# Kernel tuning notes

Measured on AMD Instinct MI355X. Metric: run time of the kernel, lower is better.

Reference implementation:

```python
import jax, jax.numpy as jnp
import numpy as np

H = 512

def setup_inputs() -> dict:
    key = jax.random.key(0)
    k1, k2, k3, k4 = jax.random.split(key, 4)
    B, S_dec, S_enc = 8, 2048, 2048
    encoder_output = jax.random.normal(k1, (B, S_enc, H), dtype=jnp.float32)
    decoder_output = jax.random.normal(k2, (B, S_dec, H), dtype=jnp.float32)
    # nn.Bilinear(H, H, 1): weight [1, H, H], bias [1]; init U(-1/sqrt(H), 1/sqrt(H))
    bound = 1.0 / np.sqrt(H)
    W = jax.random.uniform(k3, (1, H, H), dtype=jnp.float32, minval=-bound, maxval=bound)
    b = jax.random.uniform(k4, (1,), dtype=jnp.float32, minval=-bound, maxval=bound)
    return {"encoder_output": encoder_output, "decoder_output": decoder_output, "W": W, "b": b}

def reference(encoder_output, decoder_output, W, b):
    # Original: scores[b,d,e] = Bilinear(enc[b,e], dec[b,d]) = enc[b,e] @ W[0] @ dec[b,d] + bias
    # Computed as two GEMMs instead of expanding to [B, S_dec, S_enc, H].
    encW = jnp.einsum('beh,hg->beg', encoder_output, W[0])   # [B, S_enc, H]
    scores = jnp.einsum('beg,bdg->bde', encW, decoder_output) + b[0]  # [B, S_dec, S_enc]
    return scores
```

## Files before the change

kernel.cpp:

```cpp
#include <hip/hip_runtime.h>

typedef __attribute__((ext_vector_type(8))) short short8;
typedef __attribute__((ext_vector_type(4))) float f32x4;
typedef __attribute__((ext_vector_type(8))) unsigned short ushort8;

__device__ __forceinline__ unsigned short f2bf(float x) {
  union { float f; unsigned u; } v; v.f = x;
  unsigned r = v.u + 0x7fffu + ((v.u >> 16) & 1u);
  return (unsigned short)(r >> 16);
}

__global__ __launch_bounds__(256) void cvt_f32_bf16_kernel(
    const float* __restrict__ in, unsigned short* __restrict__ out, int n8) {
  int i = blockIdx.x * 256 + threadIdx.x;
  if (i >= n8) return;
  const float4* p = (const float4*)(in + (long)i * 8);
  float4 a = p[0], b = p[1];
  ushort8 o;
  o[0] = f2bf(a.x); o[1] = f2bf(a.y); o[2] = f2bf(a.z); o[3] = f2bf(a.w);
  o[4] = f2bf(b.x); o[5] = f2bf(b.y); o[6] = f2bf(b.z); o[7] = f2bf(b.w);
  *(ushort8*)(out + (long)i * 8) = o;
}

__global__ __launch_bounds__(256) void wt_kernel(
    const float* __restrict__ W, unsigned short* __restrict__ Wt) {
  __shared__ float s[64][65];
  int g0 = blockIdx.x * 64, h0 = blockIdx.y * 64;
  int tx = threadIdx.x & 63, ty = threadIdx.x >> 6;
#pragma unroll
  for (int rr = 0; rr < 16; ++rr) {
    int h = ty * 16 + rr;
    s[h][tx] = W[(long)(h0 + h) * 512 + g0 + tx];
  }
  __syncthreads();
#pragma unroll
  for (int rr = 0; rr < 16; ++rr) {
    int g = ty * 16 + rr;
    Wt[(long)(g0 + g) * 512 + h0 + tx] = f2bf(s[tx][g]);
  }
}

__global__ __launch_bounds__(256) void gemm1_abt(
    const unsigned short* __restrict__ A, const unsigned short* __restrict__ Bt,
    unsigned short* __restrict__ C, int M, int N, int K) {
  constexpr int BK = 32;
  __shared__ __align__(16) short As[128 * BK];
  __shared__ __align__(16) short Bs[128 * BK];
  const int tid = threadIdx.x;
  const int wave = tid >> 6, lane = tid & 63;
  const int wm = wave >> 1, wn = wave & 1;
  const unsigned short* Ab = A + (long)blockIdx.x * 128 * K;
  const unsigned short* Bb = Bt + (long)blockIdx.y * 128 * K;
  const int r = lane & 15, q = lane >> 4;

  f32x4 acc[4][4] = {};

  for (int kt = 0; kt < K; kt += BK) {
#pragma unroll
    for (int j = 0; j < 2; ++j) {
      int c = (j * 4 + wave) * 64 + lane;
      int row = c >> 2;
      int coff = (c & 3) * 8;
      __builtin_amdgcn_global_load_lds(
          (const __attribute__((address_space(1))) void*)(Ab + (long)row * K + kt + coff),
          (__attribute__((address_space(3))) void*)(As + (j * 4 + wave) * 512),
          16, 0, 0);
      __builtin_amdgcn_global_load_lds(
          (const __attribute__((address_space(1))) void*)(Bb + (long)row * K + kt + coff),
          (__attribute__((address_space(3))) void*)(Bs + (j * 4 + wave) * 512),
          16, 0, 0);
    }
    __syncthreads();

    short8 af[4], bfr[4];
#pragma unroll
    for (int m = 0; m < 4; ++m)
      af[m] = *(const short8*)&As[(wm * 64 + m * 16 + r) * BK + q * 8];
#pragma unroll
    for (int n = 0; n < 4; ++n)
      bfr[n] = *(const short8*)&Bs[(wn * 64 + n * 16 + r) * BK + q * 8];

#pragma unroll
    for (int m = 0; m < 4; ++m)
#pragma unroll
      for (int n = 0; n < 4; ++n)
        acc[m][n] = __builtin_amdgcn_mfma_f32_16x16x32_bf16(af[m], bfr[n], acc[m][n], 0, 0, 0);
    __syncthreads();
  }

  const long rowbase = (long)blockIdx.x * 128 + wm * 64;
  const long colbase = (long)blockIdx.y * 128 + wn * 64;
#pragma unroll
  for (int m = 0; m < 4; ++m)
#pragma unroll
    for (int n = 0; n < 4; ++n)
#pragma unroll
      for (int j = 0; j < 4; ++j) {
        long row = rowbase + m * 16 + q * 4 + j;
        long col = colbase + n * 16 + r;
        C[row * (long)N + col] = f2bf(acc[m][n][j]);
      }
}


#define VMCNT(n) asm volatile("s_waitcnt vmcnt(" #n ")" ::: "memory")

#define STAGE(GP, LBASE, tt, kkv)                                             \
  do {                                                                        \
    _Pragma("unroll") for (int j_ = 0; j_ < 2; ++j_) {                        \
      int c_ = w * 2 + j_;                                                    \
      __builtin_amdgcn_global_load_lds(                                       \
          (const __attribute__((address_space(1))) void*)(                    \
              (GP) + ((long)(c_ * 16 + srow)) * 512 + (tt) * 64 + (kkv) * 32 + scol), \
          (__attribute__((address_space(3))) void*)((LBASE) + (c_ << 10)),    \
          16, 0, 0);                                                          \
    }                                                                         \
  } while (0)

#define PHASE(Ac, Bc, kkv, mb, LOADB, STAGE_STMT, ENDWAIT_STMT)               \
  do {                                                                        \
    if (LOADB) {                                                              \
      _Pragma("unroll") for (int n_ = 0; n_ < 4; ++n_)                        \
        bf[kkv][n_] = *(const short8*)((Bc) + (kkv) * 16384 +                 \
                                       ((wn * 4 + n_) << 10) + lconst);       \
    }                                                                         \
    _Pragma("unroll") for (int i_ = 0; i_ < 4; ++i_)                          \
      af[i_] = *(const short8*)((Ac) + (kkv) * 16384 +                        \
                                ((wm * 8 + (mb) + i_) << 10) + lconst);       \
    STAGE_STMT;                                                               \
    __builtin_amdgcn_s_barrier();                                             \
    asm volatile("s_waitcnt lgkmcnt(0)" ::: "memory");                        \
    __builtin_amdgcn_sched_barrier(0);                                        \
    __builtin_amdgcn_s_setprio(1);                                            \
    _Pragma("unroll") for (int i_ = 0; i_ < 4; ++i_)                          \
      _Pragma("unroll") for (int n_ = 0; n_ < 4; ++n_)                        \
        acc[(mb) + i_][n_] = __builtin_amdgcn_mfma_f32_16x16x32_bf16(         \
            af[i_], bf[kkv][n_], acc[(mb) + i_][n_], 0, 0, 0);                \
    __builtin_amdgcn_s_setprio(0);                                            \
    ENDWAIT_STMT;                                                             \
    __builtin_amdgcn_s_barrier();                                             \
  } while (0)

__global__ __launch_bounds__(512, 2) void gemm2_8ph(
    const unsigned short* __restrict__ A,
    const unsigned short* __restrict__ Bt,
    float* __restrict__ C, const float* __restrict__ bias) {
  __shared__ __align__(16) char Lds[131072];
#define LDS_A(d) (Lds + (d) * 32768)
#define LDS_B(d) (Lds + 65536 + (d) * 32768)

  int flat = blockIdx.x;
  int sw = (flat & 7) * 64 + (flat >> 3);
  int z = sw >> 6, xy = sw & 63, bx = xy & 7, by = xy >> 3;

  const int tid = threadIdx.x;
  const int w = tid >> 6, lane = tid & 63;
  const int wm = w >> 2, wn = w & 3;
  const int base_r = lane & 15, q = lane >> 4;
  const int lconst = base_r * 64 + ((q * 16) ^ ((base_r & 8) << 2));
  const int srow = lane >> 2;
  const int scol = ((lane & 3) * 8) ^ (((lane >> 5) & 1) << 4);

  const unsigned short* Ab = A + ((long)z * 2048 + bx * 256) * 512;
  const unsigned short* Bb = Bt + ((long)z * 2048 + by * 256) * 512;

  f32x4 acc[8][4] = {};
  short8 af[4];
  short8 bf[2][4];

  STAGE(Ab, LDS_A(0), 0, 0);
  STAGE(Bb, LDS_B(0), 0, 0);
  STAGE(Ab, LDS_A(0) + 16384, 0, 1);
  STAGE(Bb, LDS_B(0) + 16384, 0, 1);
  VMCNT(4);
  __builtin_amdgcn_s_barrier();

  for (int t = 0; t < 7; ++t) {
    const char* Ac = LDS_A(t & 1);
    const char* Bc = LDS_B(t & 1);
    char* An = LDS_A((t + 1) & 1);
    char* Bn = LDS_B((t + 1) & 1);
    PHASE(Ac, Bc, 0, 0, true,  STAGE(Ab, An, t + 1, 0),         (void)0);
    PHASE(Ac, Bc, 0, 4, false, STAGE(Bb, Bn, t + 1, 0),         VMCNT(4));
    PHASE(Ac, Bc, 1, 0, true,  STAGE(Ab, An + 16384, t + 1, 1), (void)0);
    PHASE(Ac, Bc, 1, 4, false, STAGE(Bb, Bn + 16384, t + 1, 1), VMCNT(4));
  }
  {
    const char* Ac = LDS_A(1);
    const char* Bc = LDS_B(1);
    PHASE(Ac, Bc, 0, 0, true,  (void)0, (void)0);
    PHASE(Ac, Bc, 0, 4, false, (void)0, VMCNT(0));
    PHASE(Ac, Bc, 1, 0, true,  (void)0, (void)0);
    PHASE(Ac, Bc, 1, 4, false, (void)0, (void)0);
  }

  const float bv = bias[0];
  float* Cb = C + ((long)z * 2048 + bx * 256 + wm * 128) * 2048 + by * 256 + wn * 64;
#pragma unroll
  for (int m = 0; m < 8; ++m)
#pragma unroll
    for (int n = 0; n < 4; ++n)
#pragma unroll
      for (int j = 0; j < 4; ++j)
        Cb[(long)(m * 16 + q * 4 + j) * 2048 + n * 16 + base_r] = acc[m][n][j] + bv;
#undef LDS_A
#undef LDS_B
}

extern "C" void kernel_launch(void* const* d_in, const int* in_sizes, int n_in,
                              void* d_out, int out_size, void* d_ws, size_t ws_size,
                              hipStream_t stream) {
  const float* enc  = (const float*)d_in[0];
  const float* dec  = (const float*)d_in[1];
  const float* W    = (const float*)d_in[2];
  const float* bias = (const float*)d_in[3];
  float* out = (float*)d_out;

  constexpr int Bn = 8, S = 2048, H = 512;
  constexpr long NE = (long)Bn * S * H;

  unsigned short* enc_bf = (unsigned short*)d_ws;
  unsigned short* dec_bf = enc_bf + NE;
  unsigned short* Wt     = dec_bf + NE;
  unsigned short* encW   = Wt + (long)H * H;

  cvt_f32_bf16_kernel<<<(int)(NE / 8 / 256), 256, 0, stream>>>(enc, enc_bf, (int)(NE / 8));
  cvt_f32_bf16_kernel<<<(int)(NE / 8 / 256), 256, 0, stream>>>(dec, dec_bf, (int)(NE / 8));
  wt_kernel<<<dim3(8, 8), 256, 0, stream>>>(W, Wt);

  gemm1_abt<<<dim3((Bn * S) / 128, H / 128, 1), 256, 0, stream>>>(
      enc_bf, Wt, encW, Bn * S, H, H);

  gemm2_8ph<<<dim3(512, 1, 1), 512, 0, stream>>>(dec_bf, encW, out, bias);
}
```

Before: 91.53 us.

## Fuse encoder bf16 conversion into GEMM1 and co-launch decoder conversion blocks

GEMM1 now reads fp32 encoder rows directly, converts them to bf16 in registers and stores them to LDS, prefetching the next K slice while the MFMAs run. This removes the separate encoder conversion pass and its bf16 round trip through memory. The decoder conversion is appended as extra blocks of the same launch, which cuts one kernel launch and lets it overlap with the GEMM tiles. A block-index swizzle changes the tile order across the grid. The cost is more fp32 global traffic and conversion work inside the GEMM, plus register-path LDS stores in place of direct global-to-LDS loads for A.

```diff
diff --git a/kernel.cpp b/kernel.cpp
--- a/kernel.cpp
+++ b/kernel.cpp
@@ -8,18 +8,6 @@
   union { float f; unsigned u; } v; v.f = x;
   unsigned r = v.u + 0x7fffu + ((v.u >> 16) & 1u);
   return (unsigned short)(r >> 16);
-}
-
-__global__ __launch_bounds__(256) void cvt_f32_bf16_kernel(
-    const float* __restrict__ in, unsigned short* __restrict__ out, int n8) {
-  int i = blockIdx.x * 256 + threadIdx.x;
-  if (i >= n8) return;
-  const float4* p = (const float4*)(in + (long)i * 8);
-  float4 a = p[0], b = p[1];
-  ushort8 o;
-  o[0] = f2bf(a.x); o[1] = f2bf(a.y); o[2] = f2bf(a.z); o[3] = f2bf(a.w);
-  o[4] = f2bf(b.x); o[5] = f2bf(b.y); o[6] = f2bf(b.z); o[7] = f2bf(b.w);
-  *(ushort8*)(out + (long)i * 8) = o;
 }
 
 __global__ __launch_bounds__(256) void wt_kernel(
@@ -40,31 +28,59 @@
   }
 }
 
-__global__ __launch_bounds__(256) void gemm1_abt(
-    const unsigned short* __restrict__ A, const unsigned short* __restrict__ Bt,
-    unsigned short* __restrict__ C, int M, int N, int K) {
-  constexpr int BK = 32;
+__global__ __launch_bounds__(256) void gemm1_plus_cvtdec(
+    const float* __restrict__ enc, const unsigned short* __restrict__ Wt,
+    unsigned short* __restrict__ encW,
+    const float* __restrict__ dec, unsigned short* __restrict__ dec_bf) {
+  if (blockIdx.x >= 512) {
+    int i = (blockIdx.x - 512) * 256 + threadIdx.x;
+    const float4* p = (const float4*)(dec + (long)i * 8);
+    float4 a = p[0], b = p[1];
+    ushort8 o;
+    o[0] = f2bf(a.x); o[1] = f2bf(a.y); o[2] = f2bf(a.z); o[3] = f2bf(a.w);
+    o[4] = f2bf(b.x); o[5] = f2bf(b.y); o[6] = f2bf(b.z); o[7] = f2bf(b.w);
+    *(ushort8*)(dec_bf + (long)i * 8) = o;
+    return;
+  }
+
+  constexpr int K = 512, N = 512, BK = 32;
   __shared__ __align__(16) short As[128 * BK];
   __shared__ __align__(16) short Bs[128 * BK];
+
+  const int g = blockIdx.x;
+  const int work = (g & 7) * 64 + (g >> 3);
+  const int bxm = work >> 2, byn = work & 3;
+
   const int tid = threadIdx.x;
   const int wave = tid >> 6, lane = tid & 63;
   const int wm = wave >> 1, wn = wave & 1;
-  const unsigned short* Ab = A + (long)blockIdx.x * 128 * K;
-  const unsigned short* Bb = Bt + (long)blockIdx.y * 128 * K;
   const int r = lane & 15, q = lane >> 4;
 
+  const float* Ab = enc + (long)bxm * 128 * K;
+  const unsigned short* Bb = Wt + (long)byn * 128 * K;
+
+  const int srow = tid >> 1, shalf = tid & 1;
+  const float* arow = Ab + (long)srow * K + shalf * 16;
+
   f32x4 acc[4][4] = {};
+  float4 av[4];
+#pragma unroll
+  for (int j = 0; j < 4; ++j) av[j] = ((const float4*)arow)[j];
 
   for (int kt = 0; kt < K; kt += BK) {
+    ushort8 o0, o1;
+    o0[0] = f2bf(av[0].x); o0[1] = f2bf(av[0].y); o0[2] = f2bf(av[0].z); o0[3] = f2bf(av[0].w);
+    o0[4] = f2bf(av[1].x); o0[5] = f2bf(av[1].y); o0[6] = f2bf(av[1].z); o0[7] = f2bf(av[1].w);
+    o1[0] = f2bf(av[2].x); o1[1] = f2bf(av[2].y); o1[2] = f2bf(av[2].z); o1[3] = f2bf(av[2].w);
+    o1[4] = f2bf(av[3].x); o1[5] = f2bf(av[3].y); o1[6] = f2bf(av[3].z); o1[7] = f2bf(av[3].w);
+    *(ushort8*)&As[srow * BK + shalf * 16 + 0] = o0;
+    *(ushort8*)&As[srow * BK + shalf * 16 + 8] = o1;
+
 #pragma unroll
     for (int j = 0; j < 2; ++j) {
       int c = (j * 4 + wave) * 64 + lane;
       int row = c >> 2;
       int coff = (c & 3) * 8;
-      __builtin_amdgcn_global_load_lds(
-          (const __attribute__((address_space(1))) void*)(Ab + (long)row * K + kt + coff),
-          (__attribute__((address_space(3))) void*)(As + (j * 4 + wave) * 512),
-          16, 0, 0);
       __builtin_amdgcn_global_load_lds(
           (const __attribute__((address_space(1))) void*)(Bb + (long)row * K + kt + coff),
           (__attribute__((address_space(3))) void*)(Bs + (j * 4 + wave) * 512),
@@ -80,6 +96,12 @@
     for (int n = 0; n < 4; ++n)
       bfr[n] = *(const short8*)&Bs[(wn * 64 + n * 16 + r) * BK + q * 8];
 
+    if (kt + BK < K) {
+      const float* ap = arow + kt + BK;
+#pragma unroll
+      for (int j = 0; j < 4; ++j) av[j] = ((const float4*)ap)[j];
+    }
+
 #pragma unroll
     for (int m = 0; m < 4; ++m)
 #pragma unroll
@@ -88,8 +110,8 @@
     __syncthreads();
   }
 
-  const long rowbase = (long)blockIdx.x * 128 + wm * 64;
-  const long colbase = (long)blockIdx.y * 128 + wn * 64;
+  const long rowbase = (long)bxm * 128 + wm * 64;
+  const long colbase = (long)byn * 128 + wn * 64;
 #pragma unroll
   for (int m = 0; m < 4; ++m)
 #pragma unroll
@@ -98,7 +120,7 @@
       for (int j = 0; j < 4; ++j) {
         long row = rowbase + m * 16 + q * 4 + j;
         long col = colbase + n * 16 + r;
-        C[row * (long)N + col] = f2bf(acc[m][n][j]);
+        encW[row * (long)N + col] = f2bf(acc[m][n][j]);
       }
 }
 
@@ -219,17 +241,14 @@
   constexpr int Bn = 8, S = 2048, H = 512;
   constexpr long NE = (long)Bn * S * H;
 
-  unsigned short* enc_bf = (unsigned short*)d_ws;
-  unsigned short* dec_bf = enc_bf + NE;
+  unsigned short* dec_bf = (unsigned short*)d_ws;
   unsigned short* Wt     = dec_bf + NE;
   unsigned short* encW   = Wt + (long)H * H;
 
-  cvt_f32_bf16_kernel<<<(int)(NE / 8 / 256), 256, 0, stream>>>(enc, enc_bf, (int)(NE / 8));
-  cvt_f32_bf16_kernel<<<(int)(NE / 8 / 256), 256, 0, stream>>>(dec, dec_bf, (int)(NE / 8));
   wt_kernel<<<dim3(8, 8), 256, 0, stream>>>(W, Wt);
 
-  gemm1_abt<<<dim3((Bn * S) / 128, H / 128, 1), 256, 0, stream>>>(
-      enc_bf, Wt, encW, Bn * S, H, H);
+  gemm1_plus_cvtdec<<<dim3(512 + 4096, 1, 1), 256, 0, stream>>>(
+      enc, Wt, encW, dec, dec_bf);
 
   gemm2_8ph<<<dim3(512, 1, 1), 512, 0, stream>>>(dec_bf, encW, out, bias);
 }
```

Result: faster. 83.47 us (-8.8%).
